# Optimization experiments

Hardware: AMD Instinct MI355X
Metric: run time of the kernel (lower is better)

The kernel has to match this reference:

```python
import jax, jax.numpy as jnp
import numpy as np

D = 1024      # d_model
H = 16        # n_heads
HD = D // H   # head_dim = 64
R = 64        # rank
E = 8         # num_experts
DFF = 4096    # d_ff
B = 4
S = 1024
EPS = 1e-5
SCALE = 1.0 / (R ** 0.5)


def setup_inputs() -> dict:
    key = jax.random.key(0)
    ks = jax.random.split(key, 16)
    rn = lambda k, shape, s: jax.random.normal(k, shape, jnp.float32) * s
    return {
        "x": rn(ks[0], (B, S, D), 1.0),
        "mask": jnp.ones((B, S), jnp.int32),
        "ln1_g": jnp.ones((D,), jnp.float32), "ln1_b": jnp.zeros((D,), jnp.float32),
        "ln2_g": jnp.ones((D,), jnp.float32), "ln2_b": jnp.zeros((D,), jnp.float32),
        "qkv_u": rn(ks[1], (D, R), D ** -0.5),
        "qkv_v": rn(ks[2], (R, 3 * D), R ** -0.5),
        "qkv_b": jnp.zeros((3 * D,), jnp.float32),
        "out_u": rn(ks[3], (D, R), D ** -0.5),
        "out_v": rn(ks[4], (R, D), R ** -0.5),
        "out_b": jnp.zeros((D,), jnp.float32),
        "u_attn": rn(ks[5], (H, HD, R), HD ** -0.5),
        "v_attn": rn(ks[6], (H, R, HD), R ** -0.5),
        "gate_w": rn(ks[7], (D, E), D ** -0.5),
        "gate_b": jnp.zeros((E,), jnp.float32),
        "eu1": rn(ks[8], (E, D, R), D ** -0.5),
        "ev1": rn(ks[9], (E, R, DFF), R ** -0.5),
        "eb1": jnp.zeros((E, DFF), jnp.float32),
        "eu2": rn(ks[10], (E, DFF, R), DFF ** -0.5),
        "ev2": rn(ks[11], (E, R, D), R ** -0.5),
        "eb2": jnp.zeros((E, D), jnp.float32),
    }


def _layernorm(x, g, b):
    m = jnp.mean(x, -1, keepdims=True)
    v = jnp.var(x, -1, keepdims=True)
    return (x - m) * jax.lax.rsqrt(v + EPS) * g + b


def _attention(x, mask, qkv_u, qkv_v, qkv_b, out_u, out_v, out_b, u_attn, v_attn):
    b, s, d = x.shape
    qkv = (x @ qkv_u) @ qkv_v + qkv_b                     # [b,s,3d]
    q, k, v = jnp.split(qkv, 3, axis=-1)
    heads = lambda t: t.reshape(b, s, H, HD).transpose(0, 2, 1, 3)  # [b,h,s,hd]
    q, k, v = heads(q), heads(k), heads(v)
    q_low = jnp.einsum('bhsd,hdr->bhsr', q, u_attn)
    k_low = jnp.einsum('bhsd,hdr->bhsr', k, u_attn)
    scores = jnp.einsum('bhqr,bhkr->bhqk', q_low, k_low) * SCALE
    scores = jnp.where(mask[:, None, None, :] == 0, -jnp.inf, scores)
    attn = jax.nn.softmax(scores, axis=-1)                # dropout in eval mode = identity
    v_low = jnp.einsum('bhsd,hdr->bhsr', v, u_attn)
    ctx_low = jnp.einsum('bhqk,bhkr->bhqr', attn, v_low)
    ctx = jnp.einsum('bhqr,hrd->bhqd', ctx_low, v_attn)
    ctx = ctx.transpose(0, 2, 1, 3).reshape(b, s, d)
    return (ctx @ out_u) @ out_v + out_b


def _moe(x, gate_w, gate_b, eu1, ev1, eb1, eu2, ev2, eb2):
    b, s, d = x.shape
    xt = x.reshape(b * s, d)                               # [T,d]
    T = b * s
    logits = xt @ gate_w + gate_b                          # [T,E]
    probs = jax.nn.softmax(logits, axis=-1)
    top_p, top_i = jax.lax.top_k(probs, 2)                 # [T,2]
    top_p = top_p / jnp.sum(top_p, -1, keepdims=True)
    # combine weights as dense [T,E] (top-2 scatter)
    w = jnp.zeros((T, E), xt.dtype).at[jnp.arange(T)[:, None], top_i].add(top_p)
    # dense per-expert low-rank MLP; combine picks the top-2 contributions
    t1 = jnp.einsum('td,edr->etr', xt, eu1)                # [E,T,R]
    h = jax.nn.relu(jnp.einsum('etr,erh->eth', t1, ev1) + eb1[:, None, :])  # [E,T,DFF]
    t2 = jnp.einsum('eth,ehr->etr', h, eu2)                # [E,T,R]
    y = jnp.einsum('etr,erd->etd', t2, ev2) + eb2[:, None, :]               # [E,T,d]
    out = jnp.einsum('te,etd->td', w, y)
    return out.reshape(b, s, d)


def reference(x, mask, ln1_g, ln1_b, ln2_g, ln2_b, qkv_u, qkv_v, qkv_b,
              out_u, out_v, out_b, u_attn, v_attn, gate_w, gate_b,
              eu1, ev1, eb1, eu2, ev2, eb2):
    x = x + _attention(_layernorm(x, ln1_g, ln1_b), mask,
                       qkv_u, qkv_v, qkv_b, out_u, out_v, out_b, u_attn, v_attn)
    x = x + _moe(_layernorm(x, ln2_g, ln2_b), gate_w, gate_b,
                 eu1, ev1, eb1, eu2, ev2, eb2)
    return x
```

## Files before the change

kernel.cpp:

```cpp
#include <hip/hip_runtime.h>
#include <hip/hip_bf16.h>

typedef __hip_bfloat16 bf16;

#define DMODEL 1024
#define NHEAD 16
#define HDIM 64
#define RANK 64
#define NEXP 8
#define DF 4096
#define NBATCH 4
#define SEQ 1024
#define NTOK 4096
#define LN_EPS 1e-5f
#define ATT_SCALE 0.125f
#define PITCH 72

typedef short bf16x8 __attribute__((ext_vector_type(8)));
typedef float f32x4  __attribute__((ext_vector_type(4)));

static __device__ __forceinline__ float b2f(bf16 v){ return __bfloat162float(v); }
static __device__ __forceinline__ bf16 f2b(float v){ return __float2bfloat16(v); }
static __device__ __forceinline__ float us2f(unsigned short u){ union{unsigned int i; float f;} c; c.i=((unsigned)u)<<16; return c.f; }
static __device__ __forceinline__ unsigned short f2us(float f){ bf16 h=__float2bfloat16(f); unsigned short u; __builtin_memcpy(&u,&h,2); return u; }

static __device__ __forceinline__ int fsw(int r, int c){
  return (r<<6) + ((((c>>2) ^ ((r>>2)&15)))<<2) + (c&3);
}

static __device__ __forceinline__ float ld1(const void* p, size_t i, int f32){
  return f32 ? ((const float*)p)[i] : b2f(((const bf16*)p)[i]);
}
static __device__ __forceinline__ void ld4(const void* p, size_t i, int f32, float* o){
  if (f32){ float4 v = *(const float4*)((const float*)p + i); o[0]=v.x; o[1]=v.y; o[2]=v.z; o[3]=v.w; }
  else { ushort4 u = *(const ushort4*)((const bf16*)p + i); o[0]=us2f(u.x); o[1]=us2f(u.y); o[2]=us2f(u.z); o[3]=us2f(u.w); }
}

__global__ void detect_kernel(const void* ln1g, int* flag, int* cnt){
  if (threadIdx.x==0){ unsigned w = *(const unsigned*)ln1g; flag[0] = (w==0x3F800000u) ? 1 : 0; }
  if (threadIdx.x<NEXP) cnt[threadIdx.x]=0;
}

__global__ void __launch_bounds__(256) transpose_kernel(const void* __restrict__ in, unsigned short* __restrict__ out,
    int IR, int IC, const int* __restrict__ dflag){
  const int f32 = dflag[0];
  const int e = blockIdx.z;
  const int r0 = blockIdx.y*64, c0 = blockIdx.x*64;
  __shared__ float T[64][65];
  const int tid = threadIdx.x;
  for (int idx=tid; idx<64*64; idx+=256){
    int i=idx>>6, j=idx&63;
    T[i][j] = ld1(in, ((size_t)e*IR + r0+i)*IC + c0+j, f32);
  }
  __syncthreads();
  for (int idx=tid; idx<64*64; idx+=256){
    int jo=idx>>6, io=idx&63;
    out[((size_t)e*IC + c0+jo)*IR + r0+io] = f2us(T[io][jo]);
  }
}

__global__ void __launch_bounds__(256) prep_kernel(const void* __restrict__ qkv_v, const void* __restrict__ qkv_b,
    const void* __restrict__ u_attn, const void* __restrict__ v_attn, const void* __restrict__ out_u,
    float* __restrict__ Wfuse, float* __restrict__ biasl, float* __restrict__ Mout, const int* __restrict__ dflag){
  const int f32 = dflag[0];
  const int h = blockIdx.x; const int tid = threadIdx.x;
  __shared__ float ua[HDIM*RANK];
  __shared__ float va[RANK*HDIM];
  for (int i=tid;i<HDIM*RANK;i+=256){ ua[i]=ld1(u_attn,(size_t)h*HDIM*RANK+i,f32); va[i]=ld1(v_attn,(size_t)h*RANK*HDIM+i,f32); }
  __syncthreads();
  for (int idx=tid; idx<3*RANK*RANK; idx+=256){
    int jq=idx/(RANK*RANK), r1=(idx/RANK)%RANK, r2=idx%RANK;
    const size_t vbase = (size_t)r1*3*DMODEL + jq*DMODEL + h*HDIM;
    float a=0.f;
    for (int hd=0;hd<HDIM;++hd) a += ld1(qkv_v,vbase+hd,f32) * ua[hd*RANK + r2];
    Wfuse[(((size_t)jq*NHEAD + h)*RANK + r1)*RANK + r2] = a;
  }
  for (int idx=tid; idx<RANK*RANK; idx+=256){
    int r1=idx/RANK, r2=idx%RANK;
    float a=0.f;
    for (int hd=0;hd<HDIM;++hd) a += va[r1*HDIM+hd] * ld1(out_u,(size_t)(h*HDIM+hd)*RANK + r2,f32);
    Mout[((size_t)h*RANK + r1)*RANK + r2] = a;
  }
  for (int idx=tid; idx<3*RANK; idx+=256){
    int jq=idx/RANK, r2=idx%RANK;
    float a=0.f;
    for (int hd=0;hd<HDIM;++hd) a += ld1(qkv_b,(size_t)jq*DMODEL + h*HDIM + hd,f32) * ua[hd*RANK + r2];
    biasl[((size_t)jq*NHEAD + h)*RANK + r2] = a;
  }
}

__global__ void __launch_bounds__(256) ln1_kernel(const void* __restrict__ x, const void* __restrict__ g,
    const void* __restrict__ b, bf16* __restrict__ y, const int* __restrict__ dflag){
  const int f32 = dflag[0];
  const int t = blockIdx.x, tid = threadIdx.x;
  float v[4];
  ld4(x, (size_t)t*DMODEL + tid*4, f32, v);
  float s=v[0]+v[1]+v[2]+v[3], sq=v[0]*v[0]+v[1]*v[1]+v[2]*v[2]+v[3]*v[3];
  #pragma unroll
  for (int o=32;o;o>>=1){ s+=__shfl_down(s,o); sq+=__shfl_down(sq,o); }
  __shared__ float red[8]; __shared__ float ms[2];
  const int lane=tid&63, wv=tid>>6;
  if (!lane){ red[wv]=s; red[4+wv]=sq; }
  __syncthreads();
  if (!tid){
    float S0=red[0]+red[1]+red[2]+red[3], SQ=red[4]+red[5]+red[6]+red[7];
    float m=S0*(1.f/DMODEL); float var=SQ*(1.f/DMODEL)-m*m;
    ms[0]=m; ms[1]=rsqrtf(var+LN_EPS);
  }
  __syncthreads();
  const float m=ms[0], rs=ms[1];
  float gv[4], bv[4];
  ld4(g, (size_t)tid*4, f32, gv); ld4(b, (size_t)tid*4, f32, bv);
  ushort4 o;
  o.x=f2us((v[0]-m)*rs*gv[0]+bv[0]);
  o.y=f2us((v[1]-m)*rs*gv[1]+bv[1]);
  o.z=f2us((v[2]-m)*rs*gv[2]+bv[2]);
  o.w=f2us((v[3]-m)*rs*gv[3]+bv[3]);
  ((ushort4*)(y + (size_t)t*DMODEL))[tid]=o;
}

__global__ void __launch_bounds__(256) ln2_kernel(const float* __restrict__ x, const void* __restrict__ g,
    const void* __restrict__ b, bf16* __restrict__ y, float* __restrict__ mean, float* __restrict__ rstd,
    const int* __restrict__ dflag){
  const int f32 = dflag[0];
  const int t = blockIdx.x, tid = threadIdx.x;
  const float4 xv = ((const float4*)(x + (size_t)t*DMODEL))[tid];
  float v0=xv.x, v1=xv.y, v2=xv.z, v3=xv.w;
  float s=v0+v1+v2+v3, sq=v0*v0+v1*v1+v2*v2+v3*v3;
  #pragma unroll
  for (int o=32;o;o>>=1){ s+=__shfl_down(s,o); sq+=__shfl_down(sq,o); }
  __shared__ float red[8]; __shared__ float ms[2];
  const int lane=tid&63, wv=tid>>6;
  if (!lane){ red[wv]=s; red[4+wv]=sq; }
  __syncthreads();
  if (!tid){
    float S0=red[0]+red[1]+red[2]+red[3], SQ=red[4]+red[5]+red[6]+red[7];
    float m=S0*(1.f/DMODEL); float var=SQ*(1.f/DMODEL)-m*m;
    float r=rsqrtf(var+LN_EPS);
    ms[0]=m; ms[1]=r; mean[t]=m; rstd[t]=r;
  }
  __syncthreads();
  const float m=ms[0], rs=ms[1];
  float gv[4], bv[4];
  ld4(g, (size_t)tid*4, f32, gv); ld4(b, (size_t)tid*4, f32, bv);
  ushort4 o;
  o.x=f2us((v0-m)*rs*gv[0]+bv[0]);
  o.y=f2us((v1-m)*rs*gv[1]+bv[1]);
  o.z=f2us((v2-m)*rs*gv[2]+bv[2]);
  o.w=f2us((v3-m)*rs*gv[3]+bv[3]);
  ((ushort4*)(y + (size_t)t*DMODEL))[tid]=o;
}

__global__ void __launch_bounds__(256) qkvlow_kernel(const bf16* __restrict__ y1, const void* __restrict__ qkv_u,
    float* __restrict__ out, const int* __restrict__ dflag){
  const int f32 = dflag[0];
  __shared__ float As[64][65], Bs[64][65];
  const int t0 = blockIdx.x*64; const int tid=threadIdx.x;
  const int rg4=(tid>>4)*4, c4=(tid&15)*4;
  float acc[4][4];
  #pragma unroll
  for (int i=0;i<4;++i){ acc[i][0]=0.f; acc[i][1]=0.f; acc[i][2]=0.f; acc[i][3]=0.f; }
  for (int k0=0;k0<DMODEL;k0+=64){
    for (int idx=tid; idx<64*16; idx+=256){
      int i=idx>>4, j=(idx&15)*4;
      ushort4 u=*(const ushort4*)(y1 + (size_t)(t0+i)*DMODEL + k0 + j);
      As[i][j]=us2f(u.x); As[i][j+1]=us2f(u.y); As[i][j+2]=us2f(u.z); As[i][j+3]=us2f(u.w);
    }
    for (int idx=tid; idx<64*16; idx+=256){
      int i=idx>>4, j=(idx&15)*4;
      ld4(qkv_u, (size_t)(k0+i)*RANK + j, f32, &Bs[i][j]);
    }
    __syncthreads();
    #pragma unroll 8
    for (int k=0;k<64;++k){
      float a0=As[rg4][k],a1=As[rg4+1][k],a2=As[rg4+2][k],a3=As[rg4+3][k];
      float b0=Bs[k][c4],b1=Bs[k][c4+1],b2v=Bs[k][c4+2],b3=Bs[k][c4+3];
      acc[0][0]+=a0*b0; acc[0][1]+=a0*b1; acc[0][2]+=a0*b2v; acc[0][3]+=a0*b3;
      acc[1][0]+=a1*b0; acc[1][1]+=a1*b1; acc[1][2]+=a1*b2v; acc[1][3]+=a1*b3;
      acc[2][0]+=a2*b0; acc[2][1]+=a2*b1; acc[2][2]+=a2*b2v; acc[2][3]+=a2*b3;
      acc[3][0]+=a3*b0; acc[3][1]+=a3*b1; acc[3][2]+=a3*b2v; acc[3][3]+=a3*b3;
    }
    __syncthreads();
  }
  #pragma unroll
  for (int i=0;i<4;++i){
    float4 o4; o4.x=acc[i][0]; o4.y=acc[i][1]; o4.z=acc[i][2]; o4.w=acc[i][3];
    *(float4*)(out + (size_t)(t0+rg4+i)*RANK + c4) = o4;
  }
}

__global__ void __launch_bounds__(256) lowproj_kernel(const float* __restrict__ qlow, const float* __restrict__ Wfuse,
    const float* __restrict__ biasl, bf16* __restrict__ qkl){
  const int jbh = blockIdx.x;
  const int jq = jbh >> 6;
  const int bh = jbh & 63;
  const int bI = bh >> 4;
  const int h  = bh & 15;
  const int s0 = blockIdx.y*64;
  const int tid = threadIdx.x;
  __shared__ float As[64][65], Bs[64][65];
  const int rg4=(tid>>4)*4, c4=(tid&15)*4;
  const float* W  = Wfuse + (size_t)(jq*NHEAD + h)*RANK*RANK;
  const float* bl = biasl + (size_t)(jq*NHEAD + h)*RANK;
  float acc[4][4];
  #pragma unroll
  for (int i=0;i<4;++i){ acc[i][0]=bl[c4]; acc[i][1]=bl[c4+1]; acc[i][2]=bl[c4+2]; acc[i][3]=bl[c4+3]; }
  for (int idx=tid; idx<64*16; idx+=256){
    int i=idx>>4, j=(idx&15)*4;
    float4 v=*(const float4*)(qlow + (size_t)(bI*SEQ + s0+i)*RANK + j);
    As[i][j]=v.x; As[i][j+1]=v.y; As[i][j+2]=v.z; As[i][j+3]=v.w;
  }
  for (int idx=tid; idx<64*16; idx+=256){
    int i=idx>>4, j=(idx&15)*4;
    float4 v=*(const float4*)(W + (size_t)i*RANK + j);
    Bs[i][j]=v.x; Bs[i][j+1]=v.y; Bs[i][j+2]=v.z; Bs[i][j+3]=v.w;
  }
  __syncthreads();
  #pragma unroll 8
  for (int k=0;k<64;++k){
    float a0=As[rg4][k],a1=As[rg4+1][k],a2=As[rg4+2][k],a3=As[rg4+3][k];
    float b0=Bs[k][c4],b1=Bs[k][c4+1],b2v=Bs[k][c4+2],b3=Bs[k][c4+3];
    acc[0][0]+=a0*b0; acc[0][1]+=a0*b1; acc[0][2]+=a0*b2v; acc[0][3]+=a0*b3;
    acc[1][0]+=a1*b0; acc[1][1]+=a1*b1; acc[1][2]+=a1*b2v; acc[1][3]+=a1*b3;
    acc[2][0]+=a2*b0; acc[2][1]+=a2*b1; acc[2][2]+=a2*b2v; acc[2][3]+=a2*b3;
    acc[3][0]+=a3*b0; acc[3][1]+=a3*b1; acc[3][2]+=a3*b2v; acc[3][3]+=a3*b3;
  }
  #pragma unroll
  for (int i=0;i<4;++i){
    ushort4 o; o.x=f2us(acc[i][0]); o.y=f2us(acc[i][1]); o.z=f2us(acc[i][2]); o.w=f2us(acc[i][3]);
    *(ushort4*)(qkl + ((size_t)jbh*SEQ + s0+rg4+i)*RANK + c4) = o;
  }
}

__global__ void __launch_bounds__(256) attn_kernel(const bf16* __restrict__ qkl, const int* __restrict__ mask,
    bf16* __restrict__ ctx){
  const int bh = blockIdx.x; const int bI = bh / NHEAD;
  const int q0 = blockIdx.y * 64;
  const size_t headoff = (size_t)bh * SEQ * RANK;
  const size_t third = (size_t)NBATCH*NHEAD*SEQ*RANK;
  const bf16* Q = qkl + headoff;
  const bf16* K = qkl + third + headoff;
  const bf16* V = qkl + 2*third + headoff;
  __shared__ __align__(16) float qs[64*64];
  __shared__ __align__(16) float ks[64*64];
  __shared__ __align__(16) float ss[64*64];
  __shared__ float mS[64], lS[64], alS[64];
  __shared__ float red[4][64];
  __shared__ int mk[64];
  const int tid = threadIdx.x;
  for (int idx=tid; idx<64*16; idx+=256){
    int i=idx>>4, j=(idx&15)*4;
    ushort4 u = *(const ushort4*)(Q + (size_t)(q0+i)*RANK + j);
    f32x4 f;
    f[0]=us2f(u.x)*ATT_SCALE; f[1]=us2f(u.y)*ATT_SCALE; f[2]=us2f(u.z)*ATT_SCALE; f[3]=us2f(u.w)*ATT_SCALE;
    *(f32x4*)(qs + fsw(i,j)) = f;
  }
  if (tid<64){ mS[tid]=-1e30f; lS[tid]=0.f; }
  const int qg4=(tid>>4)*4, c4=(tid&15)*4;
  const int qrow=tid&63, rg=tid>>6;
  float acc[16];
  #pragma unroll
  for (int i=0;i<16;++i) acc[i]=0.f;
  for (int k0=0;k0<SEQ;k0+=64){
    for (int idx=tid; idx<64*16; idx+=256){
      int i=idx>>4, j=(idx&15)*4;
      ushort4 u = *(const ushort4*)(K + (size_t)(k0+i)*RANK + j);
      f32x4 f;
      f[0]=us2f(u.x); f[1]=us2f(u.y); f[2]=us2f(u.z); f[3]=us2f(u.w);
      *(f32x4*)(ks + fsw(i,j)) = f;
    }
    if (tid<64) mk[tid] = mask[(size_t)bI*SEQ + k0 + tid];
    __syncthreads();
    {
      float sacc[4][4];
      #pragma unroll
      for (int i=0;i<4;++i){ sacc[i][0]=0.f; sacc[i][1]=0.f; sacc[i][2]=0.f; sacc[i][3]=0.f; }
      #pragma unroll 4
      for (int r0=0;r0<RANK;r0+=4){
        f32x4 qf0 = *(const f32x4*)(qs + fsw(qg4+0, r0));
        f32x4 qf1 = *(const f32x4*)(qs + fsw(qg4+1, r0));
        f32x4 qf2 = *(const f32x4*)(qs + fsw(qg4+2, r0));
        f32x4 qf3 = *(const f32x4*)(qs + fsw(qg4+3, r0));
        f32x4 kf0 = *(const f32x4*)(ks + fsw(c4+0, r0));
        f32x4 kf1 = *(const f32x4*)(ks + fsw(c4+1, r0));
        f32x4 kf2 = *(const f32x4*)(ks + fsw(c4+2, r0));
        f32x4 kf3 = *(const f32x4*)(ks + fsw(c4+3, r0));
        #pragma unroll
        for (int rr=0;rr<4;++rr){
          float a0=qf0[rr],a1=qf1[rr],a2=qf2[rr],a3=qf3[rr];
          float b0=kf0[rr],b1=kf1[rr],b2v=kf2[rr],b3=kf3[rr];
          sacc[0][0]+=a0*b0; sacc[0][1]+=a0*b1; sacc[0][2]+=a0*b2v; sacc[0][3]+=a0*b3;
          sacc[1][0]+=a1*b0; sacc[1][1]+=a1*b1; sacc[1][2]+=a1*b2v; sacc[1][3]+=a1*b3;
          sacc[2][0]+=a2*b0; sacc[2][1]+=a2*b1; sacc[2][2]+=a2*b2v; sacc[2][3]+=a2*b3;
          sacc[3][0]+=a3*b0; sacc[3][1]+=a3*b1; sacc[3][2]+=a3*b2v; sacc[3][3]+=a3*b3;
        }
      }
      #pragma unroll
      for (int i=0;i<4;++i){
        f32x4 o;
        #pragma unroll
        for (int j=0;j<4;++j) o[j] = (mk[c4+j]==0) ? -1e30f : sacc[i][j];
        *(f32x4*)(ss + fsw(qg4+i, c4)) = o;
      }
    }
    __syncthreads();
    for (int idx=tid; idx<64*16; idx+=256){
      int i=idx>>4, j=(idx&15)*4;
      ushort4 u = *(const ushort4*)(V + (size_t)(k0+i)*RANK + j);
      f32x4 f;
      f[0]=us2f(u.x); f[1]=us2f(u.y); f[2]=us2f(u.z); f[3]=us2f(u.w);
      *(f32x4*)(ks + fsw(i,j)) = f;
    }
    {
      float pm=-1e30f;
      const int kb=rg*16;
      #pragma unroll
      for (int c=0;c<4;++c){
        f32x4 v = *(const f32x4*)(ss + fsw(qrow, kb+c*4));
        pm=fmaxf(pm,v[0]); pm=fmaxf(pm,v[1]); pm=fmaxf(pm,v[2]); pm=fmaxf(pm,v[3]);
      }
      red[rg][qrow]=pm;
    }
    __syncthreads();
    if (tid<64){
      float mn = fmaxf(fmaxf(red[0][tid],red[1][tid]),fmaxf(red[2][tid],red[3][tid]));
      mn = fmaxf(mn, mS[tid]);
      alS[tid] = __expf(mS[tid]-mn);
      mS[tid] = mn;
    }
    __syncthreads();
    {
      const float m = mS[qrow];
      float psum=0.f;
      const int kb=rg*16;
      #pragma unroll
      for (int c=0;c<4;++c){
        f32x4 v = *(f32x4*)(ss + fsw(qrow, kb+c*4));
        #pragma unroll
        for (int e=0;e<4;++e){ float p=__expf(v[e]-m); v[e]=p; psum+=p; }
        *(f32x4*)(ss + fsw(qrow, kb+c*4)) = v;
      }
      red[rg][qrow]=psum;
    }
    __syncthreads();
    if (tid<64) lS[tid] = lS[tid]*alS[tid] + red[0][tid]+red[1][tid]+red[2][tid]+red[3][tid];
    {
      float al0=alS[qg4], al1=alS[qg4+1], al2=alS[qg4+2], al3=alS[qg4+3];
      #pragma unroll
      for (int j=0;j<4;++j){ acc[0*4+j]*=al0; acc[1*4+j]*=al1; acc[2*4+j]*=al2; acc[3*4+j]*=al3; }
      #pragma unroll 4
      for (int kk0=0;kk0<64;kk0+=4){
        f32x4 pf0 = *(const f32x4*)(ss + fsw(qg4+0, kk0));
        f32x4 pf1 = *(const f32x4*)(ss + fsw(qg4+1, kk0));
        f32x4 pf2 = *(const f32x4*)(ss + fsw(qg4+2, kk0));
        f32x4 pf3 = *(const f32x4*)(ss + fsw(qg4+3, kk0));
        f32x4 vf0 = *(const f32x4*)(ks + fsw(kk0+0, c4));
        f32x4 vf1 = *(const f32x4*)(ks + fsw(kk0+1, c4));
        f32x4 vf2 = *(const f32x4*)(ks + fsw(kk0+2, c4));
        f32x4 vf3 = *(const f32x4*)(ks + fsw(kk0+3, c4));
        #pragma unroll
        for (int dk=0;dk<4;++dk){
          f32x4 vf = (dk==0)?vf0:((dk==1)?vf1:((dk==2)?vf2:vf3));
          float b0=vf[0],b1=vf[1],b2v=vf[2],b3=vf[3];
          float p0=pf0[dk],p1=pf1[dk],p2=pf2[dk],p3=pf3[dk];
          acc[0]+=p0*b0;  acc[1]+=p0*b1;  acc[2]+=p0*b2v;  acc[3]+=p0*b3;
          acc[4]+=p1*b0;  acc[5]+=p1*b1;  acc[6]+=p1*b2v;  acc[7]+=p1*b3;
          acc[8]+=p2*b0;  acc[9]+=p2*b1;  acc[10]+=p2*b2v; acc[11]+=p2*b3;
          acc[12]+=p3*b0; acc[13]+=p3*b1; acc[14]+=p3*b2v; acc[15]+=p3*b3;
        }
      }
    }
    __syncthreads();
  }
  #pragma unroll
  for (int i=0;i<4;++i){
    const float inv = 1.f/lS[qg4+i];
    ushort4 o;
    o.x=f2us(acc[i*4+0]*inv); o.y=f2us(acc[i*4+1]*inv); o.z=f2us(acc[i*4+2]*inv); o.w=f2us(acc[i*4+3]*inv);
    *(ushort4*)(ctx + headoff + (size_t)(q0+qg4+i)*RANK + c4) = o;
  }
}

__global__ void __launch_bounds__(256) outlow_kernel(const bf16* __restrict__ ctx, const float* __restrict__ Mout,
    float* __restrict__ outl){
  const int t0 = blockIdx.x*64; const int bI = t0/SEQ; const int s0 = t0%SEQ;
  const int tid = threadIdx.x;
  __shared__ __align__(16) float As[64*64];
  __shared__ __align__(16) float Bs[64*64];
  const int rg4=(tid>>4)*4, c4=(tid&15)*4;
  float acc[4][4];
  #pragma unroll
  for (int i=0;i<4;++i){ acc[i][0]=0.f; acc[i][1]=0.f; acc[i][2]=0.f; acc[i][3]=0.f; }
  for (int h=0;h<NHEAD;++h){
    for (int idx=tid; idx<64*16; idx+=256){
      int i=idx>>4, j=(idx&15)*4;
      ushort4 u=*(const ushort4*)(ctx + ((size_t)(bI*NHEAD+h)*SEQ + s0+i)*RANK + j);
      f32x4 f;
      f[0]=us2f(u.x); f[1]=us2f(u.y); f[2]=us2f(u.z); f[3]=us2f(u.w);
      *(f32x4*)(As + fsw(i,j)) = f;
    }
    for (int idx=tid; idx<64*16; idx+=256){
      int i=idx>>4, j=(idx&15)*4;
      f32x4 f = *(const f32x4*)(Mout + ((size_t)h*RANK + i)*RANK + j);
      *(f32x4*)(Bs + fsw(i,j)) = f;
    }
    __syncthreads();
    #pragma unroll 4
    for (int k0=0;k0<64;k0+=4){
      f32x4 af0 = *(const f32x4*)(As + fsw(rg4+0, k0));
      f32x4 af1 = *(const f32x4*)(As + fsw(rg4+1, k0));
      f32x4 af2 = *(const f32x4*)(As + fsw(rg4+2, k0));
      f32x4 af3 = *(const f32x4*)(As + fsw(rg4+3, k0));
      f32x4 bf0 = *(const f32x4*)(Bs + fsw(k0+0, c4));
      f32x4 bf1 = *(const f32x4*)(Bs + fsw(k0+1, c4));
      f32x4 bf2 = *(const f32x4*)(Bs + fsw(k0+2, c4));
      f32x4 bf3 = *(const f32x4*)(Bs + fsw(k0+3, c4));
      #pragma unroll
      for (int rr=0;rr<4;++rr){
        f32x4 bf = (rr==0)?bf0:((rr==1)?bf1:((rr==2)?bf2:bf3));
        float a0=af0[rr],a1=af1[rr],a2=af2[rr],a3=af3[rr];
        float b0=bf[0],b1=bf[1],b2v=bf[2],b3=bf[3];
        acc[0][0]+=a0*b0; acc[0][1]+=a0*b1; acc[0][2]+=a0*b2v; acc[0][3]+=a0*b3;
        acc[1][0]+=a1*b0; acc[1][1]+=a1*b1; acc[1][2]+=a1*b2v; acc[1][3]+=a1*b3;
        acc[2][0]+=a2*b0; acc[2][1]+=a2*b1; acc[2][2]+=a2*b2v; acc[2][3]+=a2*b3;
        acc[3][0]+=a3*b0; acc[3][1]+=a3*b1; acc[3][2]+=a3*b2v; acc[3][3]+=a3*b3;
      }
    }
    __syncthreads();
  }
  #pragma unroll
  for (int i=0;i<4;++i){
    float4 o4; o4.x=acc[i][0]; o4.y=acc[i][1]; o4.z=acc[i][2]; o4.w=acc[i][3];
    *(float4*)(outl + (size_t)(t0+rg4+i)*RANK + c4) = o4;
  }
}

__global__ void __launch_bounds__(256) resid1_kernel(const void* __restrict__ x, const float* __restrict__ outl,
    const void* __restrict__ out_v, const void* __restrict__ out_b, float* __restrict__ x1,
    const int* __restrict__ dflag){
  const int f32 = dflag[0];
  const int t0 = blockIdx.x*16; const int d = blockIdx.y*256 + threadIdx.x;
  __shared__ float ol[16][64];
  for (int idx=threadIdx.x; idx<16*16; idx+=256){
    int i=idx>>4, j=(idx&15)*4;
    float4 v=*(const float4*)(outl + (size_t)(t0+i)*RANK + j);
    ol[i][j]=v.x; ol[i][j+1]=v.y; ol[i][j+2]=v.z; ol[i][j+3]=v.w;
  }
  __syncthreads();
  float acc[16];
  #pragma unroll
  for (int i=0;i<16;++i) acc[i]=0.f;
  #pragma unroll 4
  for (int r=0;r<RANK;++r){
    float w = ld1(out_v, (size_t)r*DMODEL + d, f32);
    #pragma unroll
    for (int i=0;i<16;++i) acc[i] += ol[i][r]*w;
  }
  const float bv = ld1(out_b, d, f32);
  #pragma unroll
  for (int i=0;i<16;++i) x1[(size_t)(t0+i)*DMODEL + d] = acc[i] + bv + ld1(x, (size_t)(t0+i)*DMODEL + d, f32);
}

__global__ void __launch_bounds__(256) gate_kernel(const float* __restrict__ x1, const void* __restrict__ g,
    const void* __restrict__ b, const float* __restrict__ mean, const float* __restrict__ rstd,
    const void* __restrict__ gw, const void* __restrict__ gb,
    int* __restrict__ topi, float* __restrict__ topw, int* __restrict__ cnt, int* __restrict__ lst,
    const int* __restrict__ dflag){
  const int f32 = dflag[0];
  const int t=blockIdx.x, tid=threadIdx.x;
  const float m=mean[t], rs=rstd[t];
  const float4 xv = ((const float4*)(x1 + (size_t)t*DMODEL))[tid];
  float gv[4], bvv[4];
  ld4(g, (size_t)tid*4, f32, gv); ld4(b, (size_t)tid*4, f32, bvv);
  float xn[4];
  xn[0]=(xv.x-m)*rs*gv[0]+bvv[0];
  xn[1]=(xv.y-m)*rs*gv[1]+bvv[1];
  xn[2]=(xv.z-m)*rs*gv[2]+bvv[2];
  xn[3]=(xv.w-m)*rs*gv[3]+bvv[3];
  float acc[8]={0.f,0.f,0.f,0.f,0.f,0.f,0.f,0.f};
  #pragma unroll
  for (int k=0;k<4;++k){
    const int d = tid*4+k;
    float w[8];
    ld4(gw, (size_t)d*NEXP, f32, w); ld4(gw, (size_t)d*NEXP+4, f32, w+4);
    #pragma unroll
    for (int e2=0;e2<8;++e2) acc[e2]+=xn[k]*w[e2];
  }
  #pragma unroll
  for (int o=32;o;o>>=1){
    #pragma unroll
    for (int e2=0;e2<8;++e2) acc[e2]+=__shfl_down(acc[e2],o);
  }
  __shared__ float red[4][8];
  const int lane=tid&63, wv=tid>>6;
  if (!lane){
    #pragma unroll
    for (int e2=0;e2<8;++e2) red[wv][e2]=acc[e2];
  }
  __syncthreads();
  if (!tid){
    float l[8];
    #pragma unroll
    for (int e2=0;e2<8;++e2) l[e2]=red[0][e2]+red[1][e2]+red[2][e2]+red[3][e2]+ld1(gb,e2,f32);
    int e0=0;
    #pragma unroll
    for (int e2=1;e2<8;++e2) if (l[e2]>l[e0]) e0=e2;
    int e1=(e0==0)?1:0;
    #pragma unroll
    for (int e2=0;e2<8;++e2) if (e2!=e0 && l[e2]>l[e1]) e1=e2;
    float p1=__expf(l[e1]-l[e0]);
    float w0v=1.f/(1.f+p1), w1v=p1/(1.f+p1);
    topi[2*t]=e0; topi[2*t+1]=e1;
    topw[2*t]=w0v; topw[2*t+1]=w1v;
    int p=atomicAdd(&cnt[e0],1); lst[(size_t)e0*NTOK+p]=2*t;
    p=atomicAdd(&cnt[e1],1); lst[(size_t)e1*NTOK+p]=2*t+1;
  }
}

__global__ void __launch_bounds__(256) moe_mfma_kernel(const bf16* __restrict__ y2,
    const unsigned short* __restrict__ eu1T, const unsigned short* __restrict__ ev1T,
    const void* __restrict__ eb1, const unsigned short* __restrict__ eu2T,
    const int* __restrict__ cnt, const int* __restrict__ lst, float* __restrict__ t2s,
    const int* __restrict__ dflag){
  const int f32 = dflag[0];
  const int e = blockIdx.x; const int start = blockIdx.y*32;
  const int nrem = cnt[e] - start;
  if (nrem<=0) return;
  const int tid=threadIdx.x;
  __shared__ __align__(16) unsigned short SHW[128*PITCH];
  __shared__ __align__(16) unsigned short SHt1[32*PITCH];
  __shared__ __align__(16) unsigned short SHh[32*PITCH];
  __shared__ int toks[32];
  if (tid<32) toks[tid] = (tid<nrem)? lst[(size_t)e*NTOK + start + tid] : -1;
  __syncthreads();
  const int lane = tid&63, w = tid>>6;
  const int rw = w&1, ch = w>>1;
  const int ln16 = lane&15, hi8 = (lane>>4)*8, rr = (lane>>4)*4;
  unsigned short* As  = SHW;
  unsigned short* BsT = SHW + 32*PITCH;
  unsigned short* EvT = SHW;
  unsigned short* Eu2 = SHW + 64*PITCH;

  f32x4 accA[2] = {{0.f,0.f,0.f,0.f},{0.f,0.f,0.f,0.f}};
  for (int kc=0; kc<DMODEL; kc+=64){
    {
      int idx=tid;
      int i=idx>>3, jc=(idx&7)*8;
      int code = toks[i];
      if (code>=0) *(uint4*)(As + i*PITCH + jc) = *(const uint4*)(y2 + (size_t)(code>>1)*DMODEL + kc + jc);
      else *(uint4*)(As + i*PITCH + jc) = make_uint4(0,0,0,0);
    }
    #pragma unroll
    for (int it=0; it<2; ++it){
      int idx = tid + it*256;
      int i=idx>>3, jc=(idx&7)*8;
      *(uint4*)(BsT + i*PITCH + jc) = *(const uint4*)(eu1T + ((size_t)e*RANK + i)*DMODEL + kc + jc);
    }
    __syncthreads();
    #pragma unroll
    for (int ks=0; ks<2; ++ks){
      bf16x8 af = *(const bf16x8*)(As + (rw*16+ln16)*PITCH + ks*32 + hi8);
      #pragma unroll
      for (int nt=0; nt<2; ++nt){
        bf16x8 bf = *(const bf16x8*)(BsT + (ch*32+nt*16+ln16)*PITCH + ks*32 + hi8);
        accA[nt] = __builtin_amdgcn_mfma_f32_16x16x32_bf16(af, bf, accA[nt], 0, 0, 0);
      }
    }
    __syncthreads();
  }
  #pragma unroll
  for (int nt=0; nt<2; ++nt)
    #pragma unroll
    for (int r=0; r<4; ++r)
      SHt1[(rw*16 + rr + r)*PITCH + ch*32 + nt*16 + ln16] = f2us(accA[nt][r]);
  __syncthreads();

  f32x4 acc2[2] = {{0.f,0.f,0.f,0.f},{0.f,0.f,0.f,0.f}};
  for (int f0=0; f0<DF; f0+=64){
    #pragma unroll
    for (int it=0; it<2; ++it){
      int idx = tid + it*256;
      int i=idx>>3, jc=(idx&7)*8;
      *(uint4*)(EvT + i*PITCH + jc) = *(const uint4*)(ev1T + ((size_t)e*DF + f0 + i)*RANK + jc);
      *(uint4*)(Eu2 + i*PITCH + jc) = *(const uint4*)(eu2T + ((size_t)e*RANK + i)*DF + f0 + jc);
    }
    __syncthreads();
    {
      float b0 = ld1(eb1, (size_t)e*DF + f0 + ch*32 + ln16, f32);
      float b1 = ld1(eb1, (size_t)e*DF + f0 + ch*32 + 16 + ln16, f32);
      f32x4 h0 = {b0,b0,b0,b0}, h1 = {b1,b1,b1,b1};
      #pragma unroll
      for (int ks=0; ks<2; ++ks){
        bf16x8 af = *(const bf16x8*)(SHt1 + (rw*16+ln16)*PITCH + ks*32 + hi8);
        bf16x8 bf0 = *(const bf16x8*)(EvT + (ch*32+ln16)*PITCH + ks*32 + hi8);
        bf16x8 bf1 = *(const bf16x8*)(EvT + (ch*32+16+ln16)*PITCH + ks*32 + hi8);
        h0 = __builtin_amdgcn_mfma_f32_16x16x32_bf16(af, bf0, h0, 0, 0, 0);
        h1 = __builtin_amdgcn_mfma_f32_16x16x32_bf16(af, bf1, h1, 0, 0, 0);
      }
      #pragma unroll
      for (int r=0; r<4; ++r){
        SHh[(rw*16 + rr + r)*PITCH + ch*32 + ln16]      = f2us(fmaxf(h0[r], 0.f));
        SHh[(rw*16 + rr + r)*PITCH + ch*32 + 16 + ln16] = f2us(fmaxf(h1[r], 0.f));
      }
    }
    __syncthreads();
    #pragma unroll
    for (int ks=0; ks<2; ++ks){
      bf16x8 af = *(const bf16x8*)(SHh + (rw*16+ln16)*PITCH + ks*32 + hi8);
      #pragma unroll
      for (int nt=0; nt<2; ++nt){
        bf16x8 bf = *(const bf16x8*)(Eu2 + (ch*32+nt*16+ln16)*PITCH + ks*32 + hi8);
        acc2[nt] = __builtin_amdgcn_mfma_f32_16x16x32_bf16(af, bf, acc2[nt], 0, 0, 0);
      }
    }
    __syncthreads();
  }
  #pragma unroll
  for (int nt=0; nt<2; ++nt)
    #pragma unroll
    for (int r=0; r<4; ++r){
      int row = rw*16 + rr + r;
      int code = toks[row];
      if (code>=0) t2s[(size_t)code*RANK + ch*32 + nt*16 + ln16] = acc2[nt][r];
    }
}

__global__ void __launch_bounds__(256) final_kernel(const float* __restrict__ x1, const float* __restrict__ t2s,
    const int* __restrict__ topi, const float* __restrict__ topw, const void* __restrict__ ev2,
    const void* __restrict__ eb2, void* __restrict__ out, const int* __restrict__ dflag){
  const int f32 = dflag[0];
  const int t0 = blockIdx.x*8;
  const int d0 = (int)threadIdx.x*4;
  __shared__ float u[8][2][64];
  __shared__ int ei[8][2];
  __shared__ float ew[8][2];
  {
    int idx = threadIdx.x;
    int i=idx>>5, s=(idx>>4)&1, j=(idx&15)*4;
    float4 v = *(const float4*)(t2s + ((size_t)(t0+i)*2+s)*RANK + j);
    float wv = topw[(t0+i)*2+s];
    u[i][s][j]=v.x*wv; u[i][s][j+1]=v.y*wv; u[i][s][j+2]=v.z*wv; u[i][s][j+3]=v.w*wv;
  }
  if (threadIdx.x<16){ int i=threadIdx.x>>1, s=threadIdx.x&1; ei[i][s]=topi[(t0+i)*2+s]; ew[i][s]=topw[(t0+i)*2+s]; }
  __syncthreads();
  for (int i=0;i<8;++i){
    const float4 xv = *(const float4*)(x1 + (size_t)(t0+i)*DMODEL + d0);
    float acc[4] = {xv.x, xv.y, xv.z, xv.w};
    #pragma unroll
    for (int s=0;s<2;++s){
      const int e = ei[i][s]; const float wv = ew[i][s];
      float eb[4];
      ld4(eb2, (size_t)e*DMODEL + d0, f32, eb);
      #pragma unroll
      for (int c=0;c<4;++c) acc[c] += wv * eb[c];
      const size_t base = (size_t)e*RANK*DMODEL + d0;
      float a2[4] = {0.f,0.f,0.f,0.f};
      #pragma unroll 8
      for (int r=0;r<RANK;++r){
        float ev[4];
        ld4(ev2, base + (size_t)r*DMODEL, f32, ev);
        const float uu = u[i][s][r];
        a2[0] += uu*ev[0]; a2[1] += uu*ev[1]; a2[2] += uu*ev[2]; a2[3] += uu*ev[3];
      }
      #pragma unroll
      for (int c=0;c<4;++c) acc[c] += a2[c];
    }
    const size_t oidx = (size_t)(t0+i)*DMODEL + d0;
    if (f32){
      float4 o4; o4.x=acc[0]; o4.y=acc[1]; o4.z=acc[2]; o4.w=acc[3];
      *(float4*)((float*)out + oidx) = o4;
    } else {
      ushort4 o; o.x=f2us(acc[0]); o.y=f2us(acc[1]); o.z=f2us(acc[2]); o.w=f2us(acc[3]);
      *(ushort4*)((bf16*)out + oidx) = o;
    }
  }
}

extern "C" void kernel_launch(void* const* d_in, const int* in_sizes, int n_in,
                              void* d_out, int out_size, void* d_ws, size_t ws_size,
                              hipStream_t stream) {
  const void* x      = d_in[0];
  const int*  mask   = (const int*)d_in[1];
  const void* ln1_g  = d_in[2];
  const void* ln1_b  = d_in[3];
  const void* ln2_g  = d_in[4];
  const void* ln2_b  = d_in[5];
  const void* qkv_u  = d_in[6];
  const void* qkv_v  = d_in[7];
  const void* qkv_b  = d_in[8];
  const void* out_u  = d_in[9];
  const void* out_v  = d_in[10];
  const void* out_b  = d_in[11];
  const void* u_attn = d_in[12];
  const void* v_attn = d_in[13];
  const void* gate_w = d_in[14];
  const void* gate_b = d_in[15];
  const void* eu1    = d_in[16];
  const void* ev1    = d_in[17];
  const void* eb1    = d_in[18];
  const void* eu2    = d_in[19];
  const void* ev2    = d_in[20];
  const void* eb2    = d_in[21];
  (void)in_sizes; (void)n_in; (void)out_size; (void)ws_size;

  char* w = (char*)d_ws; size_t off=0;
  auto alloc=[&](size_t bytes){ size_t o=off; off=(off+bytes+255)&~(size_t)255; return o; };
  int*   flag  = (int*)  (w+alloc(256));
  float* Wfuse = (float*)(w+alloc((size_t)3*NHEAD*RANK*RANK*4));
  float* biasl = (float*)(w+alloc((size_t)3*NHEAD*RANK*4));
  float* Mout  = (float*)(w+alloc((size_t)NHEAD*RANK*RANK*4));
  float* qlow  = (float*)(w+alloc((size_t)NTOK*RANK*4));
  float* outl  = (float*)(w+alloc((size_t)NTOK*RANK*4));
  float* mean2 = (float*)(w+alloc((size_t)NTOK*4));
  float* rstd2 = (float*)(w+alloc((size_t)NTOK*4));
  int*   topi  = (int*)  (w+alloc((size_t)NTOK*2*4));
  float* topw  = (float*)(w+alloc((size_t)NTOK*2*4));
  int*   cnt   = (int*)  (w+alloc(256));
  int*   lst   = (int*)  (w+alloc((size_t)NEXP*NTOK*4));
  float* t2s   = (float*)(w+alloc((size_t)NTOK*2*RANK*4));
  unsigned short* eu1T = (unsigned short*)(w+alloc((size_t)NEXP*RANK*DMODEL*2));
  unsigned short* ev1T = (unsigned short*)(w+alloc((size_t)NEXP*DF*RANK*2));
  unsigned short* eu2T = (unsigned short*)(w+alloc((size_t)NEXP*RANK*DF*2));
  size_t regA = alloc((size_t)NBATCH*NHEAD*SEQ*RANK*2);
  bf16*  y1   = (bf16*)(w+regA);
  bf16*  ctx  = (bf16*)(w+regA);
  size_t regB = alloc((size_t)3*NBATCH*NHEAD*SEQ*RANK*2);
  bf16*  qkl  = (bf16*)(w+regB);
  float* x1   = (float*)(w+regB);
  bf16*  y2   = (bf16*)(w+alloc((size_t)NTOK*DMODEL*2));

  detect_kernel<<<1,64,0,stream>>>(ln1_g, flag, cnt);
  transpose_kernel<<<dim3(1,DMODEL/64,NEXP),256,0,stream>>>(eu1, eu1T, DMODEL, RANK, flag);
  transpose_kernel<<<dim3(DF/64,1,NEXP),256,0,stream>>>(ev1, ev1T, RANK, DF, flag);
  transpose_kernel<<<dim3(1,DF/64,NEXP),256,0,stream>>>(eu2, eu2T, DF, RANK, flag);
  prep_kernel<<<NHEAD,256,0,stream>>>(qkv_v,qkv_b,u_attn,v_attn,out_u,Wfuse,biasl,Mout,flag);
  ln1_kernel<<<NTOK,256,0,stream>>>(x,ln1_g,ln1_b,y1,flag);
  qkvlow_kernel<<<NTOK/64,256,0,stream>>>(y1,qkv_u,qlow,flag);
  lowproj_kernel<<<dim3(3*NBATCH*NHEAD, SEQ/64),256,0,stream>>>(qlow,Wfuse,biasl,qkl);
  attn_kernel<<<dim3(NBATCH*NHEAD, SEQ/64),256,0,stream>>>(qkl,mask,ctx);
  outlow_kernel<<<NTOK/64,256,0,stream>>>(ctx,Mout,outl);
  resid1_kernel<<<dim3(NTOK/16, DMODEL/256),256,0,stream>>>(x,outl,out_v,out_b,x1,flag);
  ln2_kernel<<<NTOK,256,0,stream>>>(x1,ln2_g,ln2_b,y2,mean2,rstd2,flag);
  gate_kernel<<<NTOK,256,0,stream>>>(x1,ln2_g,ln2_b,mean2,rstd2,gate_w,gate_b,topi,topw,cnt,lst,flag);
  moe_mfma_kernel<<<dim3(NEXP, NTOK/32),256,0,stream>>>(y2,eu1T,ev1T,eb1,eu2T,cnt,lst,t2s,flag);
  final_kernel<<<NTOK/8,256,0,stream>>>(x1,t2s,topi,topw,ev2,eb2,d_out,flag);
}
```

Before: 1.004 ms.

## Split MoE d_ff loop across blocks with reduce kernel; store attention tiles as bf16

The MoE MFMA kernel gains a third grid dimension that splits the d_ff loop into four spans. Each span writes partial rank-64 results to a new scratch buffer, and a new reduce kernel sums the four partials into t2s. This is meant to fix low block parallelism, since only about one block per 32 routed tokens was active. The cost is recomputing the first projection in every split, plus extra global traffic and one more launch. Separately, the attention kernel keeps Q, K and V tiles in shared memory as bf16 instead of fp32, converting on read and applying the scale to the scores. This halves LDS use for those tiles but adds conversion work in the inner loops.

```diff
diff --git a/kernel.cpp b/kernel.cpp
--- a/kernel.cpp
+++ b/kernel.cpp
@@ -15,6 +15,8 @@
 #define LN_EPS 1e-5f
 #define ATT_SCALE 0.125f
 #define PITCH 72
+#define NSPLIT 4
+#define FSPAN (DF/NSPLIT)
 
 typedef short bf16x8 __attribute__((ext_vector_type(8)));
 typedef float f32x4  __attribute__((ext_vector_type(4)));
@@ -241,8 +243,8 @@
   const bf16* Q = qkl + headoff;
   const bf16* K = qkl + third + headoff;
   const bf16* V = qkl + 2*third + headoff;
-  __shared__ __align__(16) float qs[64*64];
-  __shared__ __align__(16) float ks[64*64];
+  __shared__ __align__(16) unsigned short qsu[64*64];
+  __shared__ __align__(16) unsigned short kvu[64*64];
   __shared__ __align__(16) float ss[64*64];
   __shared__ float mS[64], lS[64], alS[64];
   __shared__ float red[4][64];
@@ -250,10 +252,7 @@
   const int tid = threadIdx.x;
   for (int idx=tid; idx<64*16; idx+=256){
     int i=idx>>4, j=(idx&15)*4;
-    ushort4 u = *(const ushort4*)(Q + (size_t)(q0+i)*RANK + j);
-    f32x4 f;
-    f[0]=us2f(u.x)*ATT_SCALE; f[1]=us2f(u.y)*ATT_SCALE; f[2]=us2f(u.z)*ATT_SCALE; f[3]=us2f(u.w)*ATT_SCALE;
-    *(f32x4*)(qs + fsw(i,j)) = f;
+    *(ushort4*)(qsu + fsw(i,j)) = *(const ushort4*)(Q + (size_t)(q0+i)*RANK + j);
   }
   if (tid<64){ mS[tid]=-1e30f; lS[tid]=0.f; }
   const int qg4=(tid>>4)*4, c4=(tid&15)*4;
@@ -264,10 +263,7 @@
   for (int k0=0;k0<SEQ;k0+=64){
     for (int idx=tid; idx<64*16; idx+=256){
       int i=idx>>4, j=(idx&15)*4;
-      ushort4 u = *(const ushort4*)(K + (size_t)(k0+i)*RANK + j);
-      f32x4 f;
-      f[0]=us2f(u.x); f[1]=us2f(u.y); f[2]=us2f(u.z); f[3]=us2f(u.w);
-      *(f32x4*)(ks + fsw(i,j)) = f;
+      *(ushort4*)(kvu + fsw(i,j)) = *(const ushort4*)(K + (size_t)(k0+i)*RANK + j);
     }
     if (tid<64) mk[tid] = mask[(size_t)bI*SEQ + k0 + tid];
     __syncthreads();
@@ -277,18 +273,27 @@
       for (int i=0;i<4;++i){ sacc[i][0]=0.f; sacc[i][1]=0.f; sacc[i][2]=0.f; sacc[i][3]=0.f; }
       #pragma unroll 4
       for (int r0=0;r0<RANK;r0+=4){
-        f32x4 qf0 = *(const f32x4*)(qs + fsw(qg4+0, r0));
-        f32x4 qf1 = *(const f32x4*)(qs + fsw(qg4+1, r0));
-        f32x4 qf2 = *(const f32x4*)(qs + fsw(qg4+2, r0));
-        f32x4 qf3 = *(const f32x4*)(qs + fsw(qg4+3, r0));
-        f32x4 kf0 = *(const f32x4*)(ks + fsw(c4+0, r0));
-        f32x4 kf1 = *(const f32x4*)(ks + fsw(c4+1, r0));
-        f32x4 kf2 = *(const f32x4*)(ks + fsw(c4+2, r0));
-        f32x4 kf3 = *(const f32x4*)(ks + fsw(c4+3, r0));
+        ushort4 qu0 = *(const ushort4*)(qsu + fsw(qg4+0, r0));
+        ushort4 qu1 = *(const ushort4*)(qsu + fsw(qg4+1, r0));
+        ushort4 qu2 = *(const ushort4*)(qsu + fsw(qg4+2, r0));
+        ushort4 qu3 = *(const ushort4*)(qsu + fsw(qg4+3, r0));
+        ushort4 ku0 = *(const ushort4*)(kvu + fsw(c4+0, r0));
+        ushort4 ku1 = *(const ushort4*)(kvu + fsw(c4+1, r0));
+        ushort4 ku2 = *(const ushort4*)(kvu + fsw(c4+2, r0));
+        ushort4 ku3 = *(const ushort4*)(kvu + fsw(c4+3, r0));
+        float qa[4][4], kb[4][4];
+        qa[0][0]=us2f(qu0.x); qa[0][1]=us2f(qu0.y); qa[0][2]=us2f(qu0.z); qa[0][3]=us2f(qu0.w);
+        qa[1][0]=us2f(qu1.x); qa[1][1]=us2f(qu1.y); qa[1][2]=us2f(qu1.z); qa[1][3]=us2f(qu1.w);
+        qa[2][0]=us2f(qu2.x); qa[2][1]=us2f(qu2.y); qa[2][2]=us2f(qu2.z); qa[2][3]=us2f(qu2.w);
+        qa[3][0]=us2f(qu3.x); qa[3][1]=us2f(qu3.y); qa[3][2]=us2f(qu3.z); qa[3][3]=us2f(qu3.w);
+        kb[0][0]=us2f(ku0.x); kb[0][1]=us2f(ku0.y); kb[0][2]=us2f(ku0.z); kb[0][3]=us2f(ku0.w);
+        kb[1][0]=us2f(ku1.x); kb[1][1]=us2f(ku1.y); kb[1][2]=us2f(ku1.z); kb[1][3]=us2f(ku1.w);
+        kb[2][0]=us2f(ku2.x); kb[2][1]=us2f(ku2.y); kb[2][2]=us2f(ku2.z); kb[2][3]=us2f(ku2.w);
+        kb[3][0]=us2f(ku3.x); kb[3][1]=us2f(ku3.y); kb[3][2]=us2f(ku3.z); kb[3][3]=us2f(ku3.w);
         #pragma unroll
         for (int rr=0;rr<4;++rr){
-          float a0=qf0[rr],a1=qf1[rr],a2=qf2[rr],a3=qf3[rr];
-          float b0=kf0[rr],b1=kf1[rr],b2v=kf2[rr],b3=kf3[rr];
+          float a0=qa[0][rr],a1=qa[1][rr],a2=qa[2][rr],a3=qa[3][rr];
+          float b0=kb[0][rr],b1=kb[1][rr],b2v=kb[2][rr],b3=kb[3][rr];
           sacc[0][0]+=a0*b0; sacc[0][1]+=a0*b1; sacc[0][2]+=a0*b2v; sacc[0][3]+=a0*b3;
           sacc[1][0]+=a1*b0; sacc[1][1]+=a1*b1; sacc[1][2]+=a1*b2v; sacc[1][3]+=a1*b3;
           sacc[2][0]+=a2*b0; sacc[2][1]+=a2*b1; sacc[2][2]+=a2*b2v; sacc[2][3]+=a2*b3;
@@ -299,17 +304,14 @@
       for (int i=0;i<4;++i){
         f32x4 o;
         #pragma unroll
-        for (int j=0;j<4;++j) o[j] = (mk[c4+j]==0) ? -1e30f : sacc[i][j];
+        for (int j=0;j<4;++j) o[j] = (mk[c4+j]==0) ? -1e30f : sacc[i][j]*ATT_SCALE;
         *(f32x4*)(ss + fsw(qg4+i, c4)) = o;
       }
     }
     __syncthreads();
     for (int idx=tid; idx<64*16; idx+=256){
       int i=idx>>4, j=(idx&15)*4;
-      ushort4 u = *(const ushort4*)(V + (size_t)(k0+i)*RANK + j);
-      f32x4 f;
-      f[0]=us2f(u.x); f[1]=us2f(u.y); f[2]=us2f(u.z); f[3]=us2f(u.w);
-      *(f32x4*)(ks + fsw(i,j)) = f;
+      *(ushort4*)(kvu + fsw(i,j)) = *(const ushort4*)(V + (size_t)(k0+i)*RANK + j);
     }
     {
       float pm=-1e30f;
@@ -354,14 +356,18 @@
         f32x4 pf1 = *(const f32x4*)(ss + fsw(qg4+1, kk0));
         f32x4 pf2 = *(const f32x4*)(ss + fsw(qg4+2, kk0));
         f32x4 pf3 = *(const f32x4*)(ss + fsw(qg4+3, kk0));
-        f32x4 vf0 = *(const f32x4*)(ks + fsw(kk0+0, c4));
-        f32x4 vf1 = *(const f32x4*)(ks + fsw(kk0+1, c4));
-        f32x4 vf2 = *(const f32x4*)(ks + fsw(kk0+2, c4));
-        f32x4 vf3 = *(const f32x4*)(ks + fsw(kk0+3, c4));
+        ushort4 vu0 = *(const ushort4*)(kvu + fsw(kk0+0, c4));
+        ushort4 vu1 = *(const ushort4*)(kvu + fsw(kk0+1, c4));
+        ushort4 vu2 = *(const ushort4*)(kvu + fsw(kk0+2, c4));
+        ushort4 vu3 = *(const ushort4*)(kvu + fsw(kk0+3, c4));
+        float vb[4][4];
+        vb[0][0]=us2f(vu0.x); vb[0][1]=us2f(vu0.y); vb[0][2]=us2f(vu0.z); vb[0][3]=us2f(vu0.w);
+        vb[1][0]=us2f(vu1.x); vb[1][1]=us2f(vu1.y); vb[1][2]=us2f(vu1.z); vb[1][3]=us2f(vu1.w);
+        vb[2][0]=us2f(vu2.x); vb[2][1]=us2f(vu2.y); vb[2][2]=us2f(vu2.z); vb[2][3]=us2f(vu2.w);
+        vb[3][0]=us2f(vu3.x); vb[3][1]=us2f(vu3.y); vb[3][2]=us2f(vu3.z); vb[3][3]=us2f(vu3.w);
         #pragma unroll
         for (int dk=0;dk<4;++dk){
-          f32x4 vf = (dk==0)?vf0:((dk==1)?vf1:((dk==2)?vf2:vf3));
-          float b0=vf[0],b1=vf[1],b2v=vf[2],b3=vf[3];
+          float b0=vb[dk][0],b1=vb[dk][1],b2v=vb[dk][2],b3=vb[dk][3];
           float p0=pf0[dk],p1=pf1[dk],p2=pf2[dk],p3=pf3[dk];
           acc[0]+=p0*b0;  acc[1]+=p0*b1;  acc[2]+=p0*b2v;  acc[3]+=p0*b3;
           acc[4]+=p1*b0;  acc[5]+=p1*b1;  acc[6]+=p1*b2v;  acc[7]+=p1*b3;
@@ -520,10 +526,11 @@
 __global__ void __launch_bounds__(256) moe_mfma_kernel(const bf16* __restrict__ y2,
     const unsigned short* __restrict__ eu1T, const unsigned short* __restrict__ ev1T,
     const void* __restrict__ eb1, const unsigned short* __restrict__ eu2T,
-    const int* __restrict__ cnt, const int* __restrict__ lst, float* __restrict__ t2s,
+    const int* __restrict__ cnt, const int* __restrict__ lst, float* __restrict__ t2p,
     const int* __restrict__ dflag){
   const int f32 = dflag[0];
   const int e = blockIdx.x; const int start = blockIdx.y*32;
+  const int split = blockIdx.z;
   const int nrem = cnt[e] - start;
   if (nrem<=0) return;
   const int tid=threadIdx.x;
@@ -576,7 +583,8 @@
   __syncthreads();
 
   f32x4 acc2[2] = {{0.f,0.f,0.f,0.f},{0.f,0.f,0.f,0.f}};
-  for (int f0=0; f0<DF; f0+=64){
+  const int fbeg = split*FSPAN;
+  for (int f0=fbeg; f0<fbeg+FSPAN; f0+=64){
     #pragma unroll
     for (int it=0; it<2; ++it){
       int idx = tid + it*256;
@@ -621,8 +629,23 @@
     for (int r=0; r<4; ++r){
       int row = rw*16 + rr + r;
       int code = toks[row];
-      if (code>=0) t2s[(size_t)code*RANK + ch*32 + nt*16 + ln16] = acc2[nt][r];
-    }
+      if (code>=0) t2p[((size_t)split*NTOK*2 + code)*RANK + ch*32 + nt*16 + ln16] = acc2[nt][r];
+    }
+}
+
+__global__ void __launch_bounds__(256) moe_reduce_kernel(const float* __restrict__ t2p, float* __restrict__ t2s){
+  const size_t N = (size_t)NTOK*2*RANK;
+  const size_t i4 = ((size_t)blockIdx.x*256 + threadIdx.x)*4;
+  float4 a = *(const float4*)(t2p + i4);
+  float4 b = *(const float4*)(t2p + N + i4);
+  float4 c = *(const float4*)(t2p + 2*N + i4);
+  float4 d = *(const float4*)(t2p + 3*N + i4);
+  float4 o;
+  o.x = ((a.x + b.x) + c.x) + d.x;
+  o.y = ((a.y + b.y) + c.y) + d.y;
+  o.z = ((a.z + b.z) + c.z) + d.z;
+  o.w = ((a.w + b.w) + c.w) + d.w;
+  *(float4*)(t2s + i4) = o;
 }
 
 __global__ void __launch_bounds__(256) final_kernel(const float* __restrict__ x1, const float* __restrict__ t2s,
@@ -718,6 +741,7 @@
   int*   cnt   = (int*)  (w+alloc(256));
   int*   lst   = (int*)  (w+alloc((size_t)NEXP*NTOK*4));
   float* t2s   = (float*)(w+alloc((size_t)NTOK*2*RANK*4));
+  float* t2p   = (float*)(w+alloc((size_t)NSPLIT*NTOK*2*RANK*4));
   unsigned short* eu1T = (unsigned short*)(w+alloc((size_t)NEXP*RANK*DMODEL*2));
   unsigned short* ev1T = (unsigned short*)(w+alloc((size_t)NEXP*DF*RANK*2));
   unsigned short* eu2T = (unsigned short*)(w+alloc((size_t)NEXP*RANK*DF*2));
@@ -742,6 +766,7 @@
   resid1_kernel<<<dim3(NTOK/16, DMODEL/256),256,0,stream>>>(x,outl,out_v,out_b,x1,flag);
   ln2_kernel<<<NTOK,256,0,stream>>>(x1,ln2_g,ln2_b,y2,mean2,rstd2,flag);
   gate_kernel<<<NTOK,256,0,stream>>>(x1,ln2_g,ln2_b,mean2,rstd2,gate_w,gate_b,topi,topw,cnt,lst,flag);
-  moe_mfma_kernel<<<dim3(NEXP, NTOK/32),256,0,stream>>>(y2,eu1T,ev1T,eb1,eu2T,cnt,lst,t2s,flag);
+  moe_mfma_kernel<<<dim3(NEXP, NTOK/32, NSPLIT),256,0,stream>>>(y2,eu1T,ev1T,eb1,eu2T,cnt,lst,t2p,flag);
+  moe_reduce_kernel<<<(NTOK*2*RANK/4)/256,256,0,stream>>>(t2p,t2s);
   final_kernel<<<NTOK/8,256,0,stream>>>(x1,t2s,topi,topw,ev2,eb2,d_out,flag);
 }
```

Result: no change. 994.6 us (-0.9%).
